# Optimization experiments

Measured on AMD Instinct MI355X. Metric: run time of the kernel, lower is better.

## Reference

```python
import jax, jax.numpy as jnp
from jax import lax
import numpy as np

ALPHA = 0.5   # weight of shape vs temporal component
GAMMA = 0.01  # soft-min temperature
BIG = 1e10    # finite stand-in for +inf borders (safe gradients)


def _softmin3(a, b, c, gamma):
    # -gamma * logsumexp(-x/gamma) over the three candidates
    z = jnp.stack([a, b, c], axis=0)
    return -gamma * jax.nn.logsumexp(-z / gamma, axis=0)


def _softdtw(D, gamma):
    """Soft-DTW value per problem. D: (B, N, N) cost matrix -> (B,).
    Classic DP: R[i,j] = D[i-1,j-1] + softmin(R[i-1,j-1], R[i-1,j], R[i,j-1])."""
    B, N, _ = D.shape
    # R row 0: R[0,0]=0, R[0,j>=1]=inf
    row0 = jnp.concatenate(
        [jnp.zeros((B, 1), D.dtype), jnp.full((B, N), BIG, D.dtype)], axis=1)
    left_init = jnp.full((B,), BIG, D.dtype)  # R[i,0] = inf for i>=1

    def row_step(R_prev, d_row):  # d_row: (B, N) = D[:, i-1, :]
        # per column j: diag = R_prev[j-1], up = R_prev[j], left = carry
        xs = (d_row.T, R_prev[:, :-1].T, R_prev[:, 1:].T)  # each (N, B)

        def col_step(r_left, x):
            d, r_diag, r_up = x
            r = d + _softmin3(r_diag, r_up, r_left, gamma)
            return r, r

        _, vals = lax.scan(col_step, left_init, xs)  # (N, B)
        R_row = jnp.concatenate([left_init[:, None], vals.T], axis=1)  # (B, N+1)
        return R_row, None

    R_last, _ = lax.scan(row_step, row0, jnp.transpose(D, (1, 0, 2)))
    return R_last[:, -1]  # R[N, N]


def _dilate(inp, tgt):
    B, C, N = inp.shape
    t = tgt.reshape(B * C, N)
    p = inp.reshape(B * C, N)
    # pairwise squared distances between 1-d points: D[k,i,j] = (t_i - p_j)^2
    D = (t[:, :, None] - p[:, None, :]) ** 2  # (B*C, N, N)

    # shape loss = soft-DTW value, averaged over channels
    sdtw = _softdtw(D, GAMMA)  # (B*C,)
    loss_shape = sdtw.reshape(B, C).mean(axis=1)  # (B,)

    # soft alignment path = gradient of soft-DTW w.r.t. the cost matrix
    E = jax.grad(lambda d: _softdtw(d, GAMMA).sum())(D)  # (B*C, N, N)

    # Omega[i,j] = (i - j)^2 temporal penalty
    idx = jnp.arange(1, N + 1, dtype=D.dtype)
    Omega = (idx[:, None] - idx[None, :]) ** 2  # (N, N)

    lt = jnp.sum(E * Omega, axis=(1, 2)) / (N * N)  # (B*C,)
    loss_temporal = lt.reshape(B, C).mean(axis=1)  # (B,)

    loss = (ALPHA * loss_shape + (1.0 - ALPHA) * loss_temporal).mean()
    return loss, loss_shape, loss_temporal


def setup_inputs() -> dict:
    key = jax.random.key(0)
    k1, k2 = jax.random.split(key)
    B, C, N = 64, 8, 160
    return {
        "input": jax.random.normal(k1, (B, C, N), jnp.float32),
        "target": jax.random.normal(k2, (B, C, N), jnp.float32),
    }


def reference(input, target):
    return _dilate(input, target)
```

## Files before the change

### kernel.cpp

```cpp
#include <hip/hip_runtime.h>
#include <math.h>


#define NN     160
#define BC_TOT 512
#define B_SZ   64
#define C_SZ   8
#define BIGC2  1e12f
#define SC2    12.01122405f
#define GLN2   0.0069314718056f
#define KPH    16
#define RSZ    328

__device__ __forceinline__ float fexp2(float x) {
#if __has_builtin(__builtin_amdgcn_exp2f)
    return __builtin_amdgcn_exp2f(x);
#else
    return exp2f(x);
#endif
}
__device__ __forceinline__ float flog2(float x) {
#if __has_builtin(__builtin_amdgcn_logf)
    return __builtin_amdgcn_logf(x);
#else
    return log2f(x);
#endif
}
__device__ __forceinline__ float frcp(float x) {
#if __has_builtin(__builtin_amdgcn_rcpf)
    return __builtin_amdgcn_rcpf(x);
#else
    return 1.0f / x;
#endif
}
__device__ __forceinline__ float dpp_up1_inj(float old, float x) {
    int oi = __builtin_bit_cast(int, old);
    int xi = __builtin_bit_cast(int, x);
    return __builtin_bit_cast(float,
        __builtin_amdgcn_update_dpp(oi, xi, 0x138, 0xF, 0xF, false));
}
__device__ __forceinline__ void barrier_lds() {
    __asm__ __volatile__("" ::: "memory");
    __builtin_amdgcn_s_waitcnt(0xC07F);
    __builtin_amdgcn_s_barrier();
    __asm__ __volatile__("" ::: "memory");
}

#define LOAD_WIN(c_, rgx_, rgd_, pvv_) do {                                   \
    const int dlo_ = 2 + (c_) * KPH;                                          \
    if (w > 0) {                                                              \
        const float4* q_ = (const float4*)&bRG[dlo_ - 2];                     \
        _Pragma("unroll")                                                     \
        for (int x_ = 0; x_ < 9; ++x_) {                                      \
            const float4 v4_ = q_[x_];                                        \
            rgx_[2 * x_]     = v4_.x; rgd_[2 * x_]     = v4_.y;               \
            rgx_[2 * x_ + 1] = v4_.z; rgd_[2 * x_ + 1] = v4_.w;               \
        }                                                                     \
    } else {                                                                  \
        _Pragma("unroll")                                                     \
        for (int x_ = 0; x_ < 18; ++x_) { rgx_[x_] = BIGC2; rgd_[x_] = 0.0f; }\
        if ((c_) == 0) rgx_[0] = 0.0f;           \
    }                                                                         \
    const int A_  = 192 - (64 * w + lane) + KPH * (c_);                       \
    const int sA_ = A_ & 3;                                                   \
    const float4* pq_ = (const float4*)&Pp[sA_][A_ - sA_];                    \
    _Pragma("unroll")                                                         \
    for (int x_ = 0; x_ < 4; ++x_) {                                          \
        const float4 p4_ = pq_[x_];                                           \
        pvv_[4 * x_]     = p4_.x; pvv_[4 * x_ + 1] = p4_.y;                   \
        pvv_[4 * x_ + 2] = p4_.z; pvv_[4 * x_ + 3] = p4_.w;                   \
    }                                                                         \
} while (0)

#define COMP_CHUNK(c_, rgx_, rgd_, pvv_) do {                                 \
    const int dlo_ = 2 + (c_) * KPH;                                          \
    if ((c_) == cLo) {         \
        u1 = isL0 ? rgx_[1] : BIGC2;  u2 = isL0 ? rgx_[0] : BIGC2;            \
        v1 = isL0 ? rgd_[1] : 0.0f;   v2 = isL0 ? rgd_[0] : 0.0f;             \
    }                                                                         \
    float djf_ = (float)(dlo_ - ti2);                       \
    _Pragma("unroll")                                                         \
    for (int u_ = 0; u_ < KPH; ++u_) {                                        \
        const int d_ = dlo_ + u_;                                             \
        const float mn = fminf(u2, fminf(u1, r1));                            \
        const float ed = fexp2(mn - u2);         \
        const float ev = fexp2(mn - u1);                                      \
        const float eh = fexp2(mn - r1);                                      \
        const float ss = ed + ev + eh;                              \
        const float rs = frcp(ss);                                            \
        const float dt = trS - pvv_[u_];                                      \
        const float rC = __builtin_fmaf(dt, dt, mn) - flog2(ss);              \
        const float nm = __builtin_fmaf(ed, v2,                               \
                         __builtin_fmaf(ev, v1, eh * s1));                    \
        const float rd = __builtin_fmaf(nm, rs, djf_ * djf_);                 \
        if (pub) { float2 pb; pb.x = rC; pb.y = rd; bRG[d_] = pb; }           \
        if (d_ == 2 * NN) {                                                   \
            if (w == 2 && lane == NN - 1 - 128) {         \
                sdtw[k] = rC * GLN2;                                          \
                wlt[k]  = rd * (1.0f / (NN * NN));                            \
            }                                                                 \
        }                                                                     \
        u2 = u1; u1 = dpp_up1_inj(rgx_[u_ + 2], rC);     \
        v2 = v1; v1 = dpp_up1_inj(rgd_[u_ + 2], rd);                          \
        r1 = rC; s1 = rd;                                                     \
        djf_ += 1.0f;                                                         \
    }                                                                         \
} while (0)

__global__ __launch_bounds__(64, 1)
void dtw_fwd_kernel(const float* __restrict__ input,
                    const float* __restrict__ target,
                    float* __restrict__ sdtw,
                    float* __restrict__ wlt)
{
    const int k    = blockIdx.x;
    const int lane = threadIdx.x;

    __shared__ __align__(16) float  Pp[4][520];
    __shared__ __align__(16) float2 bRG[RSZ];

    const float* tg = target + (size_t)k * NN;
    const float* pg = input  + (size_t)k * NN;
    for (int x = lane; x < 520; x += 64) {
        #pragma unroll
        for (int s = 0; s < 4; ++s) {
            const int v = x + s - 192;
            Pp[s][x] = ((unsigned)v < (unsigned)NN) ? pg[v] * SC2 : 0.0f;
        }
    }
    for (int x = lane; x < RSZ; x += 64) {
        float2 z; z.x = BIGC2; z.y = 0.0f;
        bRG[x] = z;
    }
    const float tr0 = tg[lane] * SC2;
    const float tr1 = tg[64 + lane] * SC2;
    const float tr2 = (lane < NN - 128) ? tg[128 + lane] * SC2 : 0.0f;
    barrier_lds();

    const bool isL0 = (lane == 0);

    for (int w = 0; w < 3; ++w) {
        __asm__ __volatile__("" ::: "memory");
        const int  cLo = 4 * w;
        const int  cHi = (4 * w + 13 < 19) ? 4 * w + 13 : 19;
        const bool pub = (lane == 63) && (w < 2);
        const float trS = (w == 0) ? tr0 : (w == 1) ? tr1 : tr2;
        const int  ti2 = 2 * (64 * w + lane + 1);

        float r1 = BIGC2, u1 = BIGC2, u2 = BIGC2;
        float s1 = 0.0f,  v1 = 0.0f,  v2 = 0.0f;

        float rgxA[18], rgdA[18], pvvA[16];
        float rgxB[18], rgdB[18], pvvB[16];

        LOAD_WIN(cLo, rgxA, rgdA, pvvA);
        for (int c = cLo; c <= cHi; c += 2) {
            LOAD_WIN(c + 1, rgxB, rgdB, pvvB);
            COMP_CHUNK(c, rgxA, rgdA, pvvA);
            if (c + 2 <= cHi) LOAD_WIN(c + 2, rgxA, rgdA, pvvA);
            COMP_CHUNK(c + 1, rgxB, rgdB, pvvB);
        }
    }
}

__global__ __launch_bounds__(64)
void finalize_kernel(const float* __restrict__ sdtw,
                     const float* __restrict__ wlt,
                     float* __restrict__ out)
{
    const int b = threadIdx.x;
    float ls = 0.0f, lt = 0.0f;
    #pragma unroll
    for (int c = 0; c < C_SZ; ++c) {
        ls += sdtw[b * C_SZ + c];
        lt += wlt[b * C_SZ + c];
    }
    ls *= (1.0f / C_SZ);
    lt *= (1.0f / C_SZ);
    out[1 + b]        = ls;
    out[1 + B_SZ + b] = lt;
    float v = 0.5f * ls + 0.5f * lt;
    #pragma unroll
    for (int o = 32; o > 0; o >>= 1) v += __shfl_down(v, o);
    if (b == 0) out[0] = v * (1.0f / B_SZ);
}

extern "C" void kernel_launch(void* const* d_in, const int* in_sizes, int n_in,
                              void* d_out, int out_size, void* d_ws, size_t ws_size,
                              hipStream_t stream) {
    const float* input  = (const float*)d_in[0];
    const float* target = (const float*)d_in[1];
    float* out = (float*)d_out;

    float* sdtw = (float*)d_ws;
    float* wlt  = sdtw + BC_TOT;

    dtw_fwd_kernel<<<BC_TOT, 64, 0, stream>>>(input, target, sdtw, wlt);
    finalize_kernel<<<1, 64, 0, stream>>>(sdtw, wlt, out);
}
```

Before: 111.6 us.

## Map three consecutive DTW rows per lane in a single wavefront sweep

Replaces the three-pass wavefront (one row per lane per pass, with the boundary row handed between passes through LDS) with a single skewed sweep where each lane owns three consecutive rows and the dependency flows lane to lane through DPP shifts. This removes the LDS publish/reload of boundary rows and the serial restart between the three passes. The diagonal count rises from about three separate partial sweeps to one sweep of about 319 steps, each doing three cells per lane. The per-step dependency chain is longer because rows 1 and 2 depend on the same step's row 0 and 1 results within a lane.

```diff
diff --git a/kernel.cpp b/kernel.cpp
--- a/kernel.cpp
+++ b/kernel.cpp
@@ -9,8 +9,6 @@
 #define BIGC2  1e12f
 #define SC2    12.01122405f
 #define GLN2   0.0069314718056f
-#define KPH    16
-#define RSZ    328
 
 __device__ __forceinline__ float fexp2(float x) {
 #if __has_builtin(__builtin_amdgcn_exp2f)
@@ -39,72 +37,57 @@
     return __builtin_bit_cast(float,
         __builtin_amdgcn_update_dpp(oi, xi, 0x138, 0xF, 0xF, false));
 }
-__device__ __forceinline__ void barrier_lds() {
-    __asm__ __volatile__("" ::: "memory");
-    __builtin_amdgcn_s_waitcnt(0xC07F);
-    __builtin_amdgcn_s_barrier();
-    __asm__ __volatile__("" ::: "memory");
-}
 
-#define LOAD_WIN(c_, rgx_, rgd_, pvv_) do {                                   \
-    const int dlo_ = 2 + (c_) * KPH;                                          \
-    if (w > 0) {                                                              \
-        const float4* q_ = (const float4*)&bRG[dlo_ - 2];                     \
-        _Pragma("unroll")                                                     \
-        for (int x_ = 0; x_ < 9; ++x_) {                                      \
-            const float4 v4_ = q_[x_];                                        \
-            rgx_[2 * x_]     = v4_.x; rgd_[2 * x_]     = v4_.y;               \
-            rgx_[2 * x_ + 1] = v4_.z; rgd_[2 * x_ + 1] = v4_.w;               \
-        }                                                                     \
-    } else {                                                                  \
-        _Pragma("unroll")                                                     \
-        for (int x_ = 0; x_ < 18; ++x_) { rgx_[x_] = BIGC2; rgd_[x_] = 0.0f; }\
-        if ((c_) == 0) rgx_[0] = 0.0f;           \
-    }                                                                         \
-    const int A_  = 192 - (64 * w + lane) + KPH * (c_);                       \
-    const int sA_ = A_ & 3;                                                   \
-    const float4* pq_ = (const float4*)&Pp[sA_][A_ - sA_];                    \
-    _Pragma("unroll")                                                         \
-    for (int x_ = 0; x_ < 4; ++x_) {                                          \
-        const float4 p4_ = pq_[x_];                                           \
-        pvv_[4 * x_]     = p4_.x; pvv_[4 * x_ + 1] = p4_.y;                   \
-        pvv_[4 * x_ + 2] = p4_.z; pvv_[4 * x_ + 3] = p4_.w;                   \
-    }                                                                         \
-} while (0)
-
-#define COMP_CHUNK(c_, rgx_, rgd_, pvv_) do {                                 \
-    const int dlo_ = 2 + (c_) * KPH;                                          \
-    if ((c_) == cLo) {         \
-        u1 = isL0 ? rgx_[1] : BIGC2;  u2 = isL0 ? rgx_[0] : BIGC2;            \
-        v1 = isL0 ? rgd_[1] : 0.0f;   v2 = isL0 ? rgd_[0] : 0.0f;             \
-    }                                                                         \
-    float djf_ = (float)(dlo_ - ti2);                       \
-    _Pragma("unroll")                                                         \
-    for (int u_ = 0; u_ < KPH; ++u_) {                                        \
-        const int d_ = dlo_ + u_;                                             \
-        const float mn = fminf(u2, fminf(u1, r1));                            \
-        const float ed = fexp2(mn - u2);         \
-        const float ev = fexp2(mn - u1);                                      \
-        const float eh = fexp2(mn - r1);                                      \
-        const float ss = ed + ev + eh;                              \
-        const float rs = frcp(ss);                                            \
-        const float dt = trS - pvv_[u_];                                      \
-        const float rC = __builtin_fmaf(dt, dt, mn) - flog2(ss);              \
-        const float nm = __builtin_fmaf(ed, v2,                               \
-                         __builtin_fmaf(ev, v1, eh * s1));                    \
-        const float rd = __builtin_fmaf(nm, rs, djf_ * djf_);                 \
-        if (pub) { float2 pb; pb.x = rC; pb.y = rd; bRG[d_] = pb; }           \
-        if (d_ == 2 * NN) {                                                   \
-            if (w == 2 && lane == NN - 1 - 128) {         \
-                sdtw[k] = rC * GLN2;                                          \
-                wlt[k]  = rd * (1.0f / (NN * NN));                            \
-            }                                                                 \
-        }                                                                     \
-        u2 = u1; u1 = dpp_up1_inj(rgx_[u_ + 2], rC);     \
-        v2 = v1; v1 = dpp_up1_inj(rgd_[u_ + 2], rd);                          \
-        r1 = rC; s1 = rd;                                                     \
-        djf_ += 1.0f;                                                         \
-    }                                                                         \
+#define STEP(PV0) do {                                                        \
+                   \
+    const float mn0 = fminf(b0, fminf(a0, r0));                               \
+    const float ed0 = fexp2(mn0 - b0);           \
+    const float ev0 = fexp2(mn0 - a0);                                        \
+    const float eh0 = fexp2(mn0 - r0);                                        \
+    const float ss0 = ed0 + ev0 + eh0;                                        \
+    const float rs0 = frcp(ss0);                                              \
+    const float dt0 = trS0 - (PV0);                                           \
+    const float n0  = __builtin_fmaf(dt0, dt0, mn0) - flog2(ss0);             \
+    const float nm0 = __builtin_fmaf(ed0, bd0,                                \
+                      __builtin_fmaf(ev0, ad0, eh0 * g0));                    \
+    const float om0 = dj0 * dj0;                                              \
+    const float nd0 = __builtin_fmaf(nm0, rs0, om0);                          \
+                                \
+    const float mn1 = fminf(b1, fminf(a1, r1));                               \
+    const float ed1 = fexp2(mn1 - b1);                                        \
+    const float ev1 = fexp2(mn1 - a1);                                        \
+    const float eh1 = fexp2(mn1 - r1);                                        \
+    const float ss1 = ed1 + ev1 + eh1;                                        \
+    const float rs1 = frcp(ss1);                                              \
+    const float dt1 = trS1 - pva;                                             \
+    const float n1  = __builtin_fmaf(dt1, dt1, mn1) - flog2(ss1);             \
+    const float nm1 = __builtin_fmaf(ed1, bd1,                                \
+                      __builtin_fmaf(ev1, ad1, eh1 * g1));                    \
+    const float dj1 = dj0 - 2.0f;                                             \
+    const float nd1 = __builtin_fmaf(nm1, rs1, dj1 * dj1);                    \
+                                \
+    const float mn2 = fminf(b2, fminf(a2, r2));                               \
+    const float ed2 = fexp2(mn2 - b2);                                        \
+    const float ev2 = fexp2(mn2 - a2);                                        \
+    const float eh2 = fexp2(mn2 - r2);                                        \
+    const float ss2 = ed2 + ev2 + eh2;                                        \
+    const float rs2 = frcp(ss2);                                              \
+    const float dt2 = trS2 - pvb;                                             \
+    const float n2  = __builtin_fmaf(dt2, dt2, mn2) - flog2(ss2);             \
+    const float nm2 = __builtin_fmaf(ed2, bd2,                                \
+                      __builtin_fmaf(ev2, ad2, eh2 * g2));                    \
+    const float dj2 = dj0 - 4.0f;                                             \
+    const float nd2 = __builtin_fmaf(nm2, rs2, dj2 * dj2);                    \
+                   \
+    b2 = a2;  bd2 = ad2;  a2 = n1;  ad2 = nd1;                                \
+    b1 = a1;  bd1 = ad1;  a1 = n0;  ad1 = nd0;                                \
+    b0 = a0;  bd0 = ad0;                                                      \
+    a0  = dpp_up1_inj(BIGC2, n2);              \
+    ad0 = dpp_up1_inj(0.0f,  nd2);            \
+    r0 = n0; r1 = n1; r2 = n2;                                                \
+    g0 = nd0; g1 = nd1; g2 = nd2;                                             \
+    pvb = pva; pva = (PV0);                                                   \
+    dj0 += 1.0f;                                                              \
 } while (0)
 
 __global__ __launch_bounds__(64, 1)
@@ -116,50 +99,52 @@
     const int k    = blockIdx.x;
     const int lane = threadIdx.x;
 
-    __shared__ __align__(16) float  Pp[4][520];
-    __shared__ __align__(16) float2 bRG[RSZ];
+    __shared__ __align__(16) float Pp[512];
 
     const float* tg = target + (size_t)k * NN;
     const float* pg = input  + (size_t)k * NN;
-    for (int x = lane; x < 520; x += 64) {
-        #pragma unroll
-        for (int s = 0; s < 4; ++s) {
-            const int v = x + s - 192;
-            Pp[s][x] = ((unsigned)v < (unsigned)NN) ? pg[v] * SC2 : 0.0f;
-        }
+    #pragma unroll
+    for (int x0 = 0; x0 < 512; x0 += 64) {
+        const int x = x0 + lane;
+        const int v = x - 192;
+        Pp[x] = ((unsigned)v < (unsigned)NN) ? pg[v] * SC2 : 0.0f;
     }
-    for (int x = lane; x < RSZ; x += 64) {
-        float2 z; z.x = BIGC2; z.y = 0.0f;
-        bRG[x] = z;
+    const int r3 = 3 * lane;
+    const float trS0 = (r3 + 0 < NN) ? tg[r3 + 0] * SC2 : 0.0f;
+    const float trS1 = (r3 + 1 < NN) ? tg[r3 + 1] * SC2 : 0.0f;
+    const float trS2 = (r3 + 2 < NN) ? tg[r3 + 2] * SC2 : 0.0f;
+    __asm__ __volatile__("" ::: "memory");
+    __builtin_amdgcn_s_waitcnt(0xC07F);
+    __asm__ __volatile__("" ::: "memory");
+
+    float r0 = BIGC2, r1 = BIGC2, r2 = BIGC2;
+    float g0 = 0.0f,  g1 = 0.0f,  g2 = 0.0f;
+    float a0 = BIGC2, a1 = BIGC2, a2 = BIGC2;
+    float ad0 = 0.0f, ad1 = 0.0f, ad2 = 0.0f;
+    float b0 = (lane == 0) ? 0.0f : BIGC2;
+    float b1 = BIGC2, b2 = BIGC2;
+    float bd0 = 0.0f, bd1 = 0.0f, bd2 = 0.0f;
+
+    float pva = 0.0f, pvb = 0.0f;
+    float dj0 = (float)(-6 * lane);
+
+    const int pb = 192 - r3;
+    float pf0 = Pp[pb + 0], pf1 = Pp[pb + 1], pf2 = Pp[pb + 2], pf3 = Pp[pb + 3];
+
+    for (int tb = 0; tb < 79; ++tb) {
+        const int tn = 4 * tb + 4;
+        const float q0 = Pp[pb + tn + 0];
+        const float q1 = Pp[pb + tn + 1];
+        const float q2 = Pp[pb + tn + 2];
+        const float q3 = Pp[pb + tn + 3];
+        STEP(pf0); STEP(pf1); STEP(pf2); STEP(pf3);
+        pf0 = q0; pf1 = q1; pf2 = q2; pf3 = q3;
     }
-    const float tr0 = tg[lane] * SC2;
-    const float tr1 = tg[64 + lane] * SC2;
-    const float tr2 = (lane < NN - 128) ? tg[128 + lane] * SC2 : 0.0f;
-    barrier_lds();
+    STEP(pf0); STEP(pf1); STEP(pf2);
 
-    const bool isL0 = (lane == 0);
-
-    for (int w = 0; w < 3; ++w) {
-        __asm__ __volatile__("" ::: "memory");
-        const int  cLo = 4 * w;
-        const int  cHi = (4 * w + 13 < 19) ? 4 * w + 13 : 19;
-        const bool pub = (lane == 63) && (w < 2);
-        const float trS = (w == 0) ? tr0 : (w == 1) ? tr1 : tr2;
-        const int  ti2 = 2 * (64 * w + lane + 1);
-
-        float r1 = BIGC2, u1 = BIGC2, u2 = BIGC2;
-        float s1 = 0.0f,  v1 = 0.0f,  v2 = 0.0f;
-
-        float rgxA[18], rgdA[18], pvvA[16];
-        float rgxB[18], rgdB[18], pvvB[16];
-
-        LOAD_WIN(cLo, rgxA, rgdA, pvvA);
-        for (int c = cLo; c <= cHi; c += 2) {
-            LOAD_WIN(c + 1, rgxB, rgdB, pvvB);
-            COMP_CHUNK(c, rgxA, rgdA, pvvA);
-            if (c + 2 <= cHi) LOAD_WIN(c + 2, rgxA, rgdA, pvvA);
-            COMP_CHUNK(c + 1, rgxB, rgdB, pvvB);
-        }
+    if (lane == 53) {
+        sdtw[k] = r0 * GLN2;
+        wlt[k]  = g0 * (1.0f / (NN * NN));
     }
 }
 
```

After: 101.4 us. -9.1%, faster.
